# Performance work log

Hardware: AMD Instinct MI355X
Metric: run time of the kernel (lower is better)

Reference implementation:

```python
import jax, jax.numpy as jnp
import numpy as np

EPS = 1e-5

def mvn(x):
    # per-(N,C) spatial mean/std normalization; torch .var is unbiased (ddof=1)
    mean = jnp.mean(x, axis=(2, 3), keepdims=True)
    var = jnp.var(x, axis=(2, 3), ddof=1, keepdims=True)
    return (x - mean) / jnp.sqrt(var + EPS)

def conv1x1(x, w, b):
    # w: [O, C] (1x1 conv collapsed), x: [B, C, H, W]
    return jnp.einsum('bchw,oc->bohw', x, w) + b[None, :, None, None]

def conv3x3(x, w, b):
    # w: [O, I, 3, 3], VALID padding (snet uses padding=0)
    y = jax.lax.conv_general_dilated(x, w, (1, 1), 'VALID',
                                     dimension_numbers=('NCHW', 'OIHW', 'NCHW'))
    return y + b[None, :, None, None]

def safe_cbrt(x):
    # pow(relu(x), 1/3) with safe gradient at 0 (forward identical)
    pos = x > 0
    return jnp.where(pos, jnp.power(jnp.where(pos, x, 1.0), 1.0 / 3.0), 0.0)

def _forward(content, style, wf_san, bf_san, wg_san, bg_san, wh_san, bh_san,
             wf_mcc, bf_mcc, wg_mcc, bg_mcc, w_fc, b_fc, w_out, b_out,
             wc1, bc1, wc2, bc2, wc3, bc3, ws1, bs1, ws2, bs2, ws3, bs3,
             w_unc, b_unc):
    B, C, H, W = content.shape
    cn = mvn(content)
    sn = mvn(style)

    # --- MCC branch: channel correlation statistic of style ---
    F_Fc = conv1x1(cn, wf_mcc, bf_mcc)                      # [B,C,H,W]
    g = conv1x1(sn, wg_mcc, bg_mcc).reshape(B, C, H * W)    # [B,C,HW]
    FC_S = jnp.sum(g * g, axis=-1) / jnp.sum(g, axis=-1)    # [B,C]
    FC_S = FC_S @ w_fc.T + b_fc                             # Linear
    part1 = F_Fc * FC_S[:, :, None, None]

    # --- WCT-like covariance branch (compressed 32-dim space) ---
    Fs0 = style - jnp.mean(style, axis=(2, 3), keepdims=True)  # nor_mean
    fc_ = conv1x1(jax.nn.relu(conv1x1(jax.nn.relu(conv1x1(cn, wc1, bc1)), wc2, bc2)), wc3, bc3)  # [B,32,H,W]
    fs_ = conv1x1(jax.nn.relu(conv3x3(jax.nn.relu(conv3x3(Fs0, ws1, bs1)), ws2, bs2)), ws3, bs3)  # [B,32,H-4,W-4]
    cdim = fc_.shape[1]
    fs_flat = fs_.reshape(B, cdim, -1)                       # [B,32,hw_s]
    cov = jnp.einsum('bci,bdi->bcd', fs_flat, fs_flat) / fs_flat.shape[2]  # [B,32,32]
    out = jnp.einsum('bcd,bdi->bci', cov, fc_.reshape(B, cdim, H * W)).reshape(B, cdim, H, W)
    part2 = conv1x1(out, w_unc, b_unc)                       # [B,512,H,W]

    # --- SANet-style attention branch ---
    F_s = conv1x1(cn, wf_san, bf_san).reshape(B, C, H * W)
    G_s = conv1x1(sn, wg_san, bg_san).reshape(B, C, H * W)
    H_s = conv1x1(style, wh_san, bh_san).reshape(B, C, H * W)
    S = jax.nn.softmax(jnp.einsum('bci,bcj->bij', F_s, G_s), axis=-1)  # [B,HW,HW]
    part3 = jnp.einsum('bcj,bij->bci', H_s, S).reshape(B, C, H, W)

    p = safe_cbrt(jax.nn.relu(part1 * part2 * part3))
    return conv1x1(p, w_out, b_out) + content


def setup_inputs() -> dict:
    key = jax.random.key(0)
    B, C, H, W = 16, 512, 32, 32
    s = 0.02
    shapes = {
        'content': (B, C, H, W), 'style': (B, C, H, W),
        'wf_san': (C, C), 'bf_san': (C,), 'wg_san': (C, C), 'bg_san': (C,),
        'wh_san': (C, C), 'bh_san': (C,),
        'wf_mcc': (C, C), 'bf_mcc': (C,), 'wg_mcc': (C, C), 'bg_mcc': (C,),
        'w_fc': (C, C), 'b_fc': (C,), 'w_out': (C, C), 'b_out': (C,),
        'wc1': (256, 512), 'bc1': (256,), 'wc2': (128, 256), 'bc2': (128,),
        'wc3': (32, 128), 'bc3': (32,),
        'ws1': (256, 512, 3, 3), 'bs1': (256,), 'ws2': (128, 256, 3, 3), 'bs2': (128,),
        'ws3': (32, 128), 'bs3': (32,),
        'w_unc': (512, 32), 'b_unc': (512,),
    }
    d = {}
    for i, (name, shp) in enumerate(shapes.items()):
        k = jax.random.fold_in(key, i)
        scale = 1.0 if name in ('content', 'style') else s
        d[name] = jax.random.normal(k, shp, dtype=jnp.float32) * scale
    return d


def reference(content, style, wf_san, bf_san, wg_san, bg_san, wh_san, bh_san,
              wf_mcc, bf_mcc, wg_mcc, bg_mcc, w_fc, b_fc, w_out, b_out,
              wc1, bc1, wc2, bc2, wc3, bc3, ws1, bs1, ws2, bs2, ws3, bs3,
              w_unc, b_unc):
    return _forward(content, style, wf_san, bf_san, wg_san, bg_san, wh_san, bh_san,
                    wf_mcc, bf_mcc, wg_mcc, bg_mcc, w_fc, b_fc, w_out, b_out,
                    wc1, bc1, wc2, bc2, wc3, bc3, ws1, bs1, ws2, bs2, ws3, bs3,
                    w_unc, b_unc)
```

## Files before the change

### kernel.cpp

```cpp
#include <hip/hip_runtime.h>
#include <hip/hip_bf16.h>
#include <math.h>


typedef __attribute__((ext_vector_type(8))) short short8;
typedef __attribute__((ext_vector_type(4))) float f32x4;
typedef unsigned short us;
#define MFMA16 __builtin_amdgcn_mfma_f32_16x16x32_bf16

__device__ inline float b2f(us b) { return __uint_as_float(((unsigned)b) << 16); }
__device__ inline us f2b(float f) {
    unsigned u = __float_as_uint(f);
    return (us)((u + 0x7FFFu + ((u >> 16) & 1u)) >> 16);
}

__device__ inline double blockReduceSumD(double v, double* sh) {
    int t = threadIdx.x;
    sh[t] = v; __syncthreads();
    for (int s = blockDim.x >> 1; s > 0; s >>= 1) {
        if (t < s) sh[t] += sh[t + s];
        __syncthreads();
    }
    double r = sh[0]; __syncthreads();
    return r;
}

__global__ __launch_bounds__(256) void stats_k(const float* __restrict__ X,
                                               float* __restrict__ mean,
                                               float* __restrict__ inv, int HW) {
    __shared__ double sh[256];
    int bc = blockIdx.x;
    const float* x = X + (size_t)bc * HW;
    int t = threadIdx.x;
    float v[4];
    double s = 0.0;
    #pragma unroll
    for (int r = 0; r < 4; ++r) { v[r] = x[t + r * 256]; s += (double)v[r]; }
    double tot = blockReduceSumD(s, sh);
    double ss = 0.0;
    #pragma unroll
    for (int r = 0; r < 4; ++r) ss += (double)v[r] * (double)v[r];
    double tot2 = blockReduceSumD(ss, sh);
    if (t == 0) {
        double m = tot / HW;
        double var = (tot2 - tot * tot / HW) / (HW - 1);
        mean[bc] = (float)m;
        inv[bc] = (float)(1.0 / sqrt(var + 1e-5));
    }
}

__global__ __launch_bounds__(256) void trn_k(const float* __restrict__ X,
                                             const float* __restrict__ mean,
                                             const float* __restrict__ inv,
                                             us* __restrict__ Yn, us* __restrict__ Yc,
                                             us* __restrict__ Yr, int C, int HW) {
    __shared__ us Ln[64 * 65];
    __shared__ us Lc[64 * 65];
    __shared__ us Lr[64 * 65];
    int bz = blockIdx.z, c0 = blockIdx.y * 64, h0 = blockIdx.x * 64;
    const float* Xb = X + (size_t)bz * C * HW;
    int t = threadIdx.x;
    int cl = t >> 3, h8 = (t & 7) * 8;
    #pragma unroll
    for (int half = 0; half < 2; ++half) {
        int c = cl + half * 32;
        int gc = c0 + c;
        float m = mean[bz * C + gc], iv = inv[bz * C + gc];
        const float4* s4 = (const float4*)&Xb[(size_t)gc * HW + h0 + h8];
        float4 f0 = s4[0], f1 = s4[1];
        float vv[8] = {f0.x, f0.y, f0.z, f0.w, f1.x, f1.y, f1.z, f1.w};
        #pragma unroll
        for (int i = 0; i < 8; ++i) {
            int li = c * 65 + h8 + i;
            if (Yn) Ln[li] = f2b((vv[i] - m) * iv);
            if (Yc) Lc[li] = f2b(vv[i] - m);
            if (Yr) Lr[li] = f2b(vv[i]);
        }
    }
    __syncthreads();
    int hl = t >> 3, c8 = (t & 7) * 8;
    #pragma unroll
    for (int half = 0; half < 2; ++half) {
        int hh = hl + half * 32;
        size_t off = ((size_t)bz * HW + h0 + hh) * (size_t)C + c0 + c8;
        us tmp[8];
        if (Yn) {
            #pragma unroll
            for (int i = 0; i < 8; ++i) tmp[i] = Ln[(c8 + i) * 65 + hh];
            *(uint4*)&Yn[off] = *(const uint4*)tmp;
        }
        if (Yc) {
            #pragma unroll
            for (int i = 0; i < 8; ++i) tmp[i] = Lc[(c8 + i) * 65 + hh];
            *(uint4*)&Yc[off] = *(const uint4*)tmp;
        }
        if (Yr) {
            #pragma unroll
            for (int i = 0; i < 8; ++i) tmp[i] = Lr[(c8 + i) * 65 + hh];
            *(uint4*)&Yr[off] = *(const uint4*)tmp;
        }
    }
}

template <typename TE>
__device__ inline void stage16(const TE* __restrict__ src, bool valid, us* dst) {
    us tmp[16];
    if (valid) {
        if constexpr (sizeof(TE) == 2) {
            uint4 a = ((const uint4*)src)[0], b = ((const uint4*)src)[1];
            *(uint4*)&tmp[0] = a; *(uint4*)&tmp[8] = b;
        } else {
            const float4* s4 = (const float4*)src;
            float4 f0 = s4[0], f1 = s4[1], f2 = s4[2], f3 = s4[3];
            float vv[16] = {f0.x, f0.y, f0.z, f0.w, f1.x, f1.y, f1.z, f1.w,
                            f2.x, f2.y, f2.z, f2.w, f3.x, f3.y, f3.z, f3.w};
            #pragma unroll
            for (int i = 0; i < 16; ++i) tmp[i] = f2b(vv[i]);
        }
    } else {
        #pragma unroll
        for (int i = 0; i < 16; ++i) tmp[i] = 0;
    }
    ((uint4*)dst)[0] = *(uint4*)&tmp[0];
    ((uint4*)dst)[1] = *(uint4*)&tmp[8];
}

template <typename TAel, typename TBel, typename TOUT, int OUTT>
__global__ __launch_bounds__(256) void mf2_k(const TAel* __restrict__ A, long astride, int lda,
                                             const TBel* __restrict__ B, long bstride, int ldb,
                                             const float* __restrict__ bias,
                                             TOUT* __restrict__ Y,
                                             const float* __restrict__ add_src,
                                             int K, int M, int N, int relu) {
    __shared__ us As[2][128][40];
    __shared__ us Bs[2][128][40];
    int bz = blockIdx.z;
    int mbase = blockIdx.y * 128, nbase = blockIdx.x * 128;
    const TAel* Ab = A + (size_t)bz * astride;
    const TBel* Bb = B + (size_t)bz * bstride;
    int t = threadIdx.x;
    int row = t & 127, kh = t >> 7;
    int wave = t >> 6, lane = t & 63, lm = lane & 15, q = lane >> 4;
    int mh = (wave >> 1) * 64, nh = (wave & 1) * 64;
    int gm = mbase + row, gn = nbase + row;
    bool vm = gm < M, vn = gn < N;

    auto stage = [&](int buf, int kb) {
        stage16(Ab + (size_t)gm * lda + kb + kh * 16, vm, &As[buf][row][kh * 16]);
        stage16(Bb + (size_t)gn * ldb + kb + kh * 16, vn, &Bs[buf][row][kh * 16]);
    };

    f32x4 acc[4][4];
    #pragma unroll
    for (int i = 0; i < 4; ++i)
        #pragma unroll
        for (int j = 0; j < 4; ++j) acc[i][j] = (f32x4){0.f, 0.f, 0.f, 0.f};

    stage(0, 0);
    __syncthreads();
    int cur = 0;
    for (int kb = 0; kb < K; kb += 32) {
        if (kb + 32 < K) stage(cur ^ 1, kb + 32);
        short8 af[4], bf[4];
        #pragma unroll
        for (int i = 0; i < 4; ++i) af[i] = *(const short8*)&As[cur][mh + i * 16 + lm][q * 8];
        #pragma unroll
        for (int j = 0; j < 4; ++j) bf[j] = *(const short8*)&Bs[cur][nh + j * 16 + lm][q * 8];
        #pragma unroll
        for (int i = 0; i < 4; ++i)
            #pragma unroll
            for (int j = 0; j < 4; ++j)
                acc[i][j] = MFMA16(af[i], bf[j], acc[i][j], 0, 0, 0);
        __syncthreads();
        cur ^= 1;
    }

    #pragma unroll
    for (int i = 0; i < 4; ++i) {
        int m0 = mbase + mh + i * 16 + q * 4;
        if (m0 >= M) continue;
        float bv[4];
        #pragma unroll
        for (int r = 0; r < 4; ++r) bv[r] = bias ? bias[m0 + r] : 0.f;
        #pragma unroll
        for (int j = 0; j < 4; ++j) {
            int n = nbase + nh + j * 16 + lm;
            if (n >= N) continue;
            float v[4];
            #pragma unroll
            for (int r = 0; r < 4; ++r) {
                float x = acc[i][j][r] + bv[r];
                if (relu) x = (x > 0.f) ? x : 0.f;
                v[r] = x;
            }
            if (OUTT == 1) {
                size_t off = ((size_t)bz * N + n) * (size_t)M + m0;
                if constexpr (sizeof(TOUT) == 2) {
                    us o4[4];
                    #pragma unroll
                    for (int r = 0; r < 4; ++r) o4[r] = f2b(v[r]);
                    *(uint2*)&Y[off] = *(const uint2*)o4;
                } else {
                    float4 f4 = make_float4(v[0], v[1], v[2], v[3]);
                    *(float4*)&Y[off] = f4;
                }
            } else {
                #pragma unroll
                for (int r = 0; r < 4; ++r) {
                    size_t off = ((size_t)bz * M + m0 + r) * (size_t)N + n;
                    float x = v[r];
                    if (add_src) x += add_src[off];
                    if constexpr (sizeof(TOUT) == 2) Y[off] = f2b(x);
                    else Y[off] = x;
                }
            }
        }
    }
}

struct SBias {
    const float* bp[10];
    int moff[10];
    unsigned relu;
};
__global__ __launch_bounds__(256) void mfs_k(const us* __restrict__ A,
                                             const us* __restrict__ B, long bstride, int ldb,
                                             us* __restrict__ Y, int ldy,
                                             SBias sb, int K, int N) {
    __shared__ us As[2][128][40];
    __shared__ us Bs[2][128][40];
    int bz = blockIdx.z;
    int mbase = blockIdx.y * 128, nbase = blockIdx.x * 128;
    const us* Bb = B + (size_t)bz * bstride;
    int t = threadIdx.x;
    int row = t & 127, kh = t >> 7;
    int wave = t >> 6, lane = t & 63, lm = lane & 15, q = lane >> 4;
    int mh = (wave >> 1) * 64, nh = (wave & 1) * 64;
    int relu = (sb.relu >> blockIdx.y) & 1;
    const float* bias = sb.bp[blockIdx.y];
    int moff = sb.moff[blockIdx.y];

    auto stage = [&](int buf, int kb) {
        stage16(A + (size_t)(mbase + row) * K + kb + kh * 16, true, &As[buf][row][kh * 16]);
        stage16(Bb + (size_t)(nbase + row) * ldb + kb + kh * 16, true, &Bs[buf][row][kh * 16]);
    };

    f32x4 acc[4][4];
    #pragma unroll
    for (int i = 0; i < 4; ++i)
        #pragma unroll
        for (int j = 0; j < 4; ++j) acc[i][j] = (f32x4){0.f, 0.f, 0.f, 0.f};

    stage(0, 0);
    __syncthreads();
    int cur = 0;
    for (int kb = 0; kb < K; kb += 32) {
        if (kb + 32 < K) stage(cur ^ 1, kb + 32);
        short8 af[4], bf[4];
        #pragma unroll
        for (int i = 0; i < 4; ++i) af[i] = *(const short8*)&As[cur][mh + i * 16 + lm][q * 8];
        #pragma unroll
        for (int j = 0; j < 4; ++j) bf[j] = *(const short8*)&Bs[cur][nh + j * 16 + lm][q * 8];
        #pragma unroll
        for (int i = 0; i < 4; ++i)
            #pragma unroll
            for (int j = 0; j < 4; ++j)
                acc[i][j] = MFMA16(af[i], bf[j], acc[i][j], 0, 0, 0);
        __syncthreads();
        cur ^= 1;
    }

    #pragma unroll
    for (int i = 0; i < 4; ++i) {
        int m0 = mbase + mh + i * 16 + q * 4;
        float bv[4];
        #pragma unroll
        for (int r = 0; r < 4; ++r) bv[r] = bias[m0 - moff + r];
        #pragma unroll
        for (int j = 0; j < 4; ++j) {
            int n = nbase + nh + j * 16 + lm;
            us o4[4];
            #pragma unroll
            for (int r = 0; r < 4; ++r) {
                float x = acc[i][j][r] + bv[r];
                if (relu) x = (x > 0.f) ? x : 0.f;
                o4[r] = f2b(x);
            }
            *(uint2*)&Y[((size_t)bz * N + n) * ldy + m0] = *(const uint2*)o4;
        }
    }
}

struct CpyArg {
    const float* src[11];
    unsigned long long dstoff[11];
    int len[11];
};
__global__ __launch_bounds__(256) void wcat_k(CpyArg a, us* __restrict__ arena) {
    int seg = blockIdx.y;
    int idx = blockIdx.x * 256 + threadIdx.x;
    if (idx < a.len[seg]) arena[a.dstoff[seg] + idx] = f2b(a.src[seg][idx]);
}

__global__ __launch_bounds__(256) void reorder_wf_k(const float* __restrict__ W,
                                                    us* __restrict__ Wf, int O, int Cin) {
    int idx = blockIdx.x * 256 + threadIdx.x;
    int OT = O >> 6, KB = Cin >> 5;
    int total = OT * KB * 9 * 4 * 64;
    if (idx >= total) return;
    int lane = idx & 63;
    int f = idx >> 6;
    int i = f & 1, half = (f >> 1) & 1;
    int tf = f >> 2;
    int tap = tf % 9;
    int rest = tf / 9;
    int kb = rest % KB, ot = rest / KB;
    int o = ot * 64 + half * 32 + i * 16 + (lane & 15);
    int cb = kb * 32 + (lane >> 4) * 8;
    us v[8];
    #pragma unroll
    for (int e = 0; e < 8; ++e)
        v[e] = f2b(W[((size_t)o * Cin + cb + e) * 9 + tap]);
    *(uint4*)&Wf[(size_t)idx * 8] = *(const uint4*)v;
}

template <int PR>
__device__ inline void stage_patch(const us* __restrict__ Xb, us* __restrict__ dst,
                                   int pyb, int kb, int Cin, int IH, int IW, int t) {
    const int ITEMS = (2 * PR + 2) * 36 * 4;
    for (int i = t; i < ITEMS; i += 256) {
        int p = i >> 2, q8 = (i & 3) * 8;
        int r = p / 36, x = p - r * 36;
        int gy = pyb + r;
        uint4 v = make_uint4(0u, 0u, 0u, 0u);
        if (x < IW && gy < IH)
            v = *(const uint4*)&Xb[((size_t)(gy * IW + x)) * Cin + kb * 32 + q8];
        *(uint4*)&dst[p * 40 + q8] = v;
    }
}

template <int PR>
__global__ __launch_bounds__(256) void conv_mf4_k(const us* __restrict__ X, long xbstride,
                                                  const us* __restrict__ Wf,
                                                  const float* __restrict__ bias,
                                                  us* __restrict__ Y, long ybstride,
                                                  int Cin, int O, int IH, int IW,
                                                  int OH, int OW) {
    __shared__ us patch[2][(2 * PR + 2) * 36 * 40];
    int bz = blockIdx.z;
    int obase = blockIdx.y * 64;
    int pyb = blockIdx.x * (2 * PR);
    const us* Xb = X + (size_t)bz * xbstride;
    int t = threadIdx.x;
    int wave = t >> 6, lane = t & 63, lm = lane & 15, q = lane >> 4;
    int half = wave >> 1, rw = wave & 1;
    int KB = Cin >> 5;
    const us* Wb = Wf + (size_t)(obase >> 6) * KB * 9 * 2048;

    f32x4 acc[PR][2][2];
    #pragma unroll
    for (int pr = 0; pr < PR; ++pr)
        #pragma unroll
        for (int i = 0; i < 2; ++i)
            #pragma unroll
            for (int j = 0; j < 2; ++j) acc[pr][i][j] = (f32x4){0.f, 0.f, 0.f, 0.f};

    stage_patch<PR>(Xb, patch[0], pyb, 0, Cin, IH, IW, t);
    __syncthreads();
    int cur = 0;
    for (int kb = 0; kb < KB; ++kb) {
        if (kb + 1 < KB) stage_patch<PR>(Xb, patch[cur ^ 1], pyb, kb + 1, Cin, IH, IW, t);
        const us* Wk = Wb + (size_t)kb * 9 * 2048;
        #pragma unroll
        for (int tap = 0; tap < 9; ++tap) {
            int ky = tap / 3, kx = tap - ky * 3;
            const us* wt = Wk + tap * 2048 + half * 1024;
            short8 a0 = *(const short8*)&wt[lane * 8];
            short8 a1 = *(const short8*)&wt[512 + lane * 8];
            #pragma unroll
            for (int pr = 0; pr < PR; ++pr) {
                int prow = (pr * 2 + rw + ky) * 36;
                short8 b0 = *(const short8*)&patch[cur][(prow + lm + kx) * 40 + q * 8];
                short8 b1 = *(const short8*)&patch[cur][(prow + 16 + lm + kx) * 40 + q * 8];
                acc[pr][0][0] = MFMA16(a0, b0, acc[pr][0][0], 0, 0, 0);
                acc[pr][0][1] = MFMA16(a0, b1, acc[pr][0][1], 0, 0, 0);
                acc[pr][1][0] = MFMA16(a1, b0, acc[pr][1][0], 0, 0, 0);
                acc[pr][1][1] = MFMA16(a1, b1, acc[pr][1][1], 0, 0, 0);
            }
        }
        __syncthreads();
        cur ^= 1;
    }

    us* Yb = Y + (size_t)bz * ybstride;
    #pragma unroll
    for (int pr = 0; pr < PR; ++pr) {
        int py = pyb + pr * 2 + rw;
        if (py >= OH) continue;
        #pragma unroll
        for (int i = 0; i < 2; ++i) {
            int m0 = obase + half * 32 + i * 16 + q * 4;
            #pragma unroll
            for (int j = 0; j < 2; ++j) {
                int px = j * 16 + lm;
                if (px >= OW) continue;
                us o4[4];
                #pragma unroll
                for (int r = 0; r < 4; ++r) {
                    float v = acc[pr][i][j][r] + bias[m0 + r];
                    v = (v > 0.f) ? v : 0.f;
                    o4[r] = f2b(v);
                }
                *(uint2*)&Yb[((size_t)(py * OW + px)) * O + m0] = *(const uint2*)o4;
            }
        }
    }
}

__global__ __launch_bounds__(256) void gemm_k(const float* __restrict__ W,
                                              const float* __restrict__ X,
                                              const float* __restrict__ bias,
                                              float* __restrict__ Y,
                                              int C, int O, int N) {
    int obase = blockIdx.y * 32;
    __shared__ float As[32][33];
    __shared__ float Bs[32][33];
    int t = threadIdx.x;
    int tx = t & 15, ty = t >> 4;
    float acc00 = 0, acc01 = 0, acc10 = 0, acc11 = 0;
    for (int cb = 0; cb < C; cb += 32) {
        int k = t & 31, o0 = t >> 5;
        #pragma unroll
        for (int r = 0; r < 4; ++r) {
            int ol = o0 + r * 8;
            As[k][ol] = W[(size_t)(obase + ol) * C + cb + k];
        }
        int n0 = t & 31, k0 = t >> 5;
        #pragma unroll
        for (int r = 0; r < 4; ++r) {
            int k2 = k0 + r * 8;
            Bs[k2][n0] = (n0 < N) ? X[(size_t)(cb + k2) * N + n0] : 0.f;
        }
        __syncthreads();
        #pragma unroll
        for (int k2 = 0; k2 < 32; ++k2) {
            float a0 = As[k2][ty], a1 = As[k2][ty + 16];
            float b0 = Bs[k2][tx], b1 = Bs[k2][tx + 16];
            acc00 += a0 * b0; acc01 += a0 * b1;
            acc10 += a1 * b0; acc11 += a1 * b1;
        }
        __syncthreads();
    }
    float accs[2][2] = {{acc00, acc01}, {acc10, acc11}};
    #pragma unroll
    for (int i = 0; i < 2; ++i) {
        int o = obase + ty + i * 16;
        float bv = bias[o];
        #pragma unroll
        for (int j = 0; j < 2; ++j) {
            int n = tx + j * 16;
            if (n < N) Y[(size_t)o * N + n] = accs[i][j] + bv;
        }
    }
}

__global__ __launch_bounds__(256) void fcs3a_k(const us* __restrict__ g, int ldg,
                                               float* __restrict__ pa, int HW) {
    int b = blockIdx.x, j = blockIdx.y;
    int t = threadIdx.x;
    const us* gb = g + ((size_t)b * HW + (size_t)j * 128) * ldg + 2 * t;
    double s0 = 0.0, s1 = 0.0;
    #pragma unroll 4
    for (int hw = 0; hw < 128; ++hw) {
        unsigned u = *(const unsigned*)&gb[(size_t)hw * ldg];
        float f0 = b2f((us)(u & 0xFFFFu));
        float f1 = b2f((us)(u >> 16));
        s0 += (double)f0 * (double)f0;
        s1 += (double)f1 * (double)f1;
    }
    float2 w = make_float2((float)s0, (float)s1);
    *(float2*)&pa[((size_t)b * 8 + j) * 512 + 2 * t] = w;
}

__global__ __launch_bounds__(256) void fcs3b_k(const float* __restrict__ pa,
                                               const float* __restrict__ bg,
                                               float* __restrict__ fcs, int B, int HW) {
    int b = blockIdx.x;
    int t = threadIdx.x;
    double s0 = 0.0, s1 = 0.0;
    #pragma unroll
    for (int j = 0; j < 8; ++j) {
        float2 w = *(const float2*)&pa[((size_t)b * 8 + j) * 512 + 2 * t];
        s0 += (double)w.x; s1 += (double)w.y;
    }
    int c0 = 2 * t;
    fcs[(size_t)c0 * B + b] = (float)(s0 / ((double)HW * (double)bg[c0]));
    fcs[(size_t)(c0 + 1) * B + b] = (float)(s1 / ((double)HW * (double)bg[c0 + 1]));
}

__global__ __launch_bounds__(256) void softmax_k(const float* __restrict__ S,
                                                 us* __restrict__ P) {
    __shared__ float sh[256];
    size_t row = blockIdx.x;
    const float* r = S + row * 1024;
    us* po = P + row * 1024;
    int t = threadIdx.x;
    float v[4];
    float m = -INFINITY;
    #pragma unroll
    for (int i = 0; i < 4; ++i) { v[i] = r[t + i * 256]; m = fmaxf(m, v[i]); }
    sh[t] = m; __syncthreads();
    for (int s = 128; s > 0; s >>= 1) { if (t < s) sh[t] = fmaxf(sh[t], sh[t + s]); __syncthreads(); }
    m = sh[0]; __syncthreads();
    float sum = 0;
    #pragma unroll
    for (int i = 0; i < 4; ++i) { v[i] = expf(v[i] - m); sum += v[i]; }
    sh[t] = sum; __syncthreads();
    for (int s = 128; s > 0; s >>= 1) { if (t < s) sh[t] += sh[t + s]; __syncthreads(); }
    float inv = 1.f / sh[0]; __syncthreads();
    #pragma unroll
    for (int i = 0; i < 4; ++i) po[t + i * 256] = f2b(v[i] * inv);
}

__global__ __launch_bounds__(256) void cov2_k(const float* __restrict__ fs,
                                              float* __restrict__ cov, int Cd, int M) {
    __shared__ float Ls[196 * 36];
    int bb = blockIdx.x;
    int t = threadIdx.x;
    const float* p = fs + (size_t)bb * M * Cd;
    int c = t >> 3, d0 = (t & 7) * 4;
    float a0 = 0.f, a1 = 0.f, a2 = 0.f, a3 = 0.f;
    for (int ch = 0; ch < 4; ++ch) {
        __syncthreads();
        for (int i = t; i < 1568; i += 256) {
            int rowi = i >> 3, c4 = (i & 7) * 4;
            float4 v = *(const float4*)&p[(size_t)(ch * 196 + rowi) * Cd + c4];
            *(float4*)&Ls[rowi * 36 + c4] = v;
        }
        __syncthreads();
        for (int i = 0; i < 196; ++i) {
            float a = Ls[i * 36 + c];
            a0 += a * Ls[i * 36 + d0 + 0];
            a1 += a * Ls[i * 36 + d0 + 1];
            a2 += a * Ls[i * 36 + d0 + 2];
            a3 += a * Ls[i * 36 + d0 + 3];
        }
    }
    float invM = 1.f / (float)M;
    size_t base = ((size_t)bb * Cd + c) * Cd + d0;
    cov[base + 0] = a0 * invM;
    cov[base + 1] = a1 * invM;
    cov[base + 2] = a2 * invM;
    cov[base + 3] = a3 * invM;
}

__global__ __launch_bounds__(256) void fuse_k(const us* __restrict__ ffc, int ldf,
                                              const float* __restrict__ fc2t,
                                              const us* __restrict__ p2,
                                              const us* __restrict__ p3,
                                              us* __restrict__ out, int B, int C, int HW) {
    size_t idx = (size_t)blockIdx.x * 256 + threadIdx.x;
    size_t total = (size_t)B * C * HW;
    if (idx >= total) return;
    int c = (int)(idx & (size_t)(C - 1));
    size_t tok = idx >> 9;
    int b = (int)(idx / ((size_t)C * HW));
    float part1 = b2f(ffc[tok * ldf + c]) * fc2t[(size_t)c * B + b];
    float v = part1 * b2f(p2[idx]) * b2f(p3[idx]);
    v = (v > 0.f) ? v : 0.f;
    out[idx] = f2b(cbrtf(v));
}

extern "C" void kernel_launch(void* const* d_in, const int* in_sizes, int n_in,
                              void* d_out, int out_size, void* d_ws, size_t ws_size,
                              hipStream_t stream) {
    typedef const float* fp;
    fp content = (fp)d_in[0];
    fp style   = (fp)d_in[1];
    fp wf_san = (fp)d_in[2],  bf_san = (fp)d_in[3];
    fp wg_san = (fp)d_in[4],  bg_san = (fp)d_in[5];
    fp wh_san = (fp)d_in[6],  bh_san = (fp)d_in[7];
    fp wf_mcc = (fp)d_in[8],  bf_mcc = (fp)d_in[9];
    fp wg_mcc = (fp)d_in[10], bg_mcc = (fp)d_in[11];
    fp w_fc   = (fp)d_in[12], b_fc   = (fp)d_in[13];
    fp w_out  = (fp)d_in[14], b_out  = (fp)d_in[15];
    fp wc1 = (fp)d_in[16], bc1 = (fp)d_in[17];
    fp wc2 = (fp)d_in[18], bc2 = (fp)d_in[19];
    fp wc3 = (fp)d_in[20], bc3 = (fp)d_in[21];
    fp ws1 = (fp)d_in[22], bs1 = (fp)d_in[23];
    fp ws2 = (fp)d_in[24], bs2 = (fp)d_in[25];
    fp ws3 = (fp)d_in[26], bs3 = (fp)d_in[27];
    fp w_unc = (fp)d_in[28], b_unc = (fp)d_in[29];

    const int B = 16, C = 512, HW = 1024;
    const size_t NE = (size_t)B * C * HW;
    const long TOK = (long)C * HW;
    const size_t MB = 1u << 20;
    char* base = (char*)d_ws;

    us* cnT      = (us*)(base);
    us* snT      = (us*)(base + 16 * MB);
    us* fs0T     = (us*)(base + 32 * MB);
    us* s1       = (us*)(base + 48 * MB);
    us* s2       = (us*)(base + 56 * MB);
    float* fs_c  = (float*)(base + 60 * MB);
    float* Sbuf  = (float*)(base);
    us* cnOut    = (us*)(base + 64 * MB);
    us* snOut    = (us*)(base + 104 * MB);
    us* part3b   = (us*)(base + 104 * MB);
    us* part2b   = (us*)(base + 120 * MB);
    us* Pb       = (us*)(base + 136 * MB);
    us* t2b      = (us*)(base + 136 * MB);
    float* fc_c  = (float*)(base + 140 * MB);
    float* out32 = (float*)(base + 142 * MB);
    us* pbuf     = (us*)(base + 144 * MB);
    us* styleT   = (us*)(base + 168 * MB);
    us* Hco      = (us*)(base + 184 * MB);

    char* misc = base + 200 * MB;
    us* Wr1   = (us*)(misc);
    us* Wr2   = (us*)(misc + 2359296);
    us* arena = (us*)(misc + 2949120);
    us* Wcn   = arena;
    us* Wsn   = arena + 655360;
    us* Wh    = arena + 1179648;
    us* Wout  = arena + 1441792;
    us* Wc2   = arena + 1703936;
    us* Wc3   = arena + 1736704;
    us* Ws3   = arena + 1740800;
    us* Wunc  = arena + 1744896;
    float* pa    = (float*)(misc + 6471680);
    float* fcs   = (float*)(misc + 6733824);
    float* fc2t  = (float*)(misc + 6766592);
    float* cov   = (float*)(misc + 6799360);
    float* meanC = (float*)(misc + 6864896);
    float* invC  = (float*)(misc + 6897664);
    float* meanS = (float*)(misc + 6930432);
    float* invS  = (float*)(misc + 6963200);

    CpyArg ca;
    const float* srcs[11] = {wf_mcc, wc1, wf_san, wg_mcc, wg_san, wh_san,
                             w_out, wc2, wc3, ws3, w_unc};
    int lens[11] = {262144, 131072, 262144, 262144, 262144, 262144,
                    262144, 32768, 4096, 4096, 16384};
    unsigned long long off = 0;
    for (int i = 0; i < 11; ++i) { ca.src[i] = srcs[i]; ca.dstoff[i] = off; ca.len[i] = lens[i]; off += lens[i]; }
    wcat_k<<<dim3(1024, 11), 256, 0, stream>>>(ca, arena);
    reorder_wf_k<<<576, 256, 0, stream>>>(ws1, Wr1, 256, 512);
    reorder_wf_k<<<72, 256, 0, stream>>>(ws2, Wr2, 128, 256);

    stats_k<<<B * C, 256, 0, stream>>>(content, meanC, invC, HW);
    stats_k<<<B * C, 256, 0, stream>>>(style, meanS, invS, HW);
    trn_k<<<dim3(16, 8, 16), 256, 0, stream>>>(content, meanC, invC, cnT, nullptr, nullptr, C, HW);
    trn_k<<<dim3(16, 8, 16), 256, 0, stream>>>(style, meanS, invS, snT, fs0T, styleT, C, HW);

    conv_mf4_k<1><<<dim3(15, 4, 16), 256, 0, stream>>>(fs0T, TOK, Wr1, bs1,
                                                       s1, (long)900 * 256, 512, 256, 32, 32, 30, 30);
    conv_mf4_k<1><<<dim3(14, 2, 16), 256, 0, stream>>>(s1, (long)900 * 256, Wr2, bs2,
                                                       s2, (long)784 * 128, 256, 128, 30, 30, 28, 28);
    mf2_k<us, us, float, 1><<<dim3(7, 1, 16), 256, 0, stream>>>(
        Ws3, 0, 128, s2, (long)784 * 128, 128, bs3, fs_c, nullptr, 128, 32, 784, 0);
    cov2_k<<<B, 256, 0, stream>>>(fs_c, cov, 32, 784);

    {
        SBias sb;
        for (int y = 0; y < 4; ++y) { sb.bp[y] = bf_mcc; sb.moff[y] = 0; }
        for (int y = 4; y < 6; ++y) { sb.bp[y] = bc1; sb.moff[y] = 512; }
        for (int y = 6; y < 10; ++y) { sb.bp[y] = bf_san; sb.moff[y] = 768; }
        sb.relu = 0x030u;
        mfs_k<<<dim3(8, 10, 16), 256, 0, stream>>>(Wcn, cnT, TOK, 512, cnOut, 1280, sb, 512, 1024);
    }

    {
        SBias sb;
        for (int y = 0; y < 4; ++y) { sb.bp[y] = bg_mcc; sb.moff[y] = 0; }
        for (int y = 4; y < 8; ++y) { sb.bp[y] = bg_san; sb.moff[y] = 512; }
        for (int y = 8; y < 10; ++y) { sb.bp[y] = bg_mcc; sb.moff[y] = 0; }
        sb.relu = 0u;
        mfs_k<<<dim3(8, 8, 16), 256, 0, stream>>>(Wsn, snT, TOK, 512, snOut, 1024, sb, 512, 1024);
    }

    fcs3a_k<<<dim3(B, 8), 256, 0, stream>>>(snOut, 1024, pa, HW);
    fcs3b_k<<<B, 256, 0, stream>>>(pa, bg_mcc, fcs, B, HW);
    gemm_k<<<dim3(1, 16, 1), 256, 0, stream>>>(w_fc, fcs, b_fc, fc2t, 512, 512, 16);

    mf2_k<us, us, us, 0><<<dim3(8, 4, 16), 256, 0, stream>>>(
        Wh, 0, 512, styleT, TOK, 512, bh_san, Hco, nullptr, 512, 512, 1024, 0);

    mf2_k<us, us, float, 0><<<dim3(8, 8, 16), 256, 0, stream>>>(
        cnOut + 768, (long)1024 * 1280, 1280, snOut + 512, (long)1024 * 1024, 1024,
        nullptr, Sbuf, nullptr, 512, 1024, 1024, 0);
    softmax_k<<<B * HW, 256, 0, stream>>>(Sbuf, Pb);

    mf2_k<us, us, us, 0><<<dim3(4, 8, 16), 256, 0, stream>>>(
        Pb, (long)1024 * 1024, 1024, Hco, TOK, 1024, nullptr, part3b, nullptr, 1024, 1024, 512, 0);

    mf2_k<us, us, us, 1><<<dim3(8, 1, 16), 256, 0, stream>>>(
        Wc2, 0, 256, cnOut + 512, (long)1024 * 1280, 1280, bc2, t2b, nullptr, 256, 128, 1024, 1);
    mf2_k<us, us, float, 1><<<dim3(8, 1, 16), 256, 0, stream>>>(
        Wc3, 0, 128, t2b, (long)1024 * 128, 128, bc3, fc_c, nullptr, 128, 32, 1024, 0);

    mf2_k<float, float, float, 1><<<dim3(8, 1, 16), 256, 0, stream>>>(
        cov, 1024, 32, fc_c, (long)1024 * 32, 32, nullptr, out32, nullptr, 32, 32, 1024, 0);
    mf2_k<us, float, us, 1><<<dim3(8, 4, 16), 256, 0, stream>>>(
        Wunc, 0, 32, out32, (long)1024 * 32, 32, b_unc, part2b, nullptr, 32, 512, 1024, 0);

    fuse_k<<<(unsigned)((NE + 255) / 256), 256, 0, stream>>>(
        cnOut, 1280, fc2t, part2b, part3b, pbuf, B, C, HW);

    mf2_k<us, us, float, 0><<<dim3(8, 4, 16), 256, 0, stream>>>(
        Wout, 0, 512, pbuf, TOK, 512, b_out, (float*)d_out, content, 512, 512, 1024, 0);
}
```

Measured before the change: 769.4 us.

## Fuse softmax into PV GEMM with fp16 scores and XCD-aware block swizzle

Attention scores are now stored as fp16 instead of fp32. A lightweight wave-per-row kernel computes the row max and inverse sum, and the exponentiation and normalization move into the A-staging step of the PV GEMM, so the separate softmax pass and the bf16 probability buffer go away. All MFMA GEMM and conv kernels also remap block IDs so that consecutive tiles land on the same XCD, aiming for better L2 locality. The costs are recomputing expf for every A tile in each of the 4 N-column blocks, and fp16 range and precision risk on the raw scores.

```diff
diff --git a/kernel.cpp b/kernel.cpp
--- a/kernel.cpp
+++ b/kernel.cpp
@@ -1,5 +1,6 @@
 #include <hip/hip_runtime.h>
 #include <hip/hip_bf16.h>
+#include <hip/hip_fp16.h>
 #include <math.h>
 
 
@@ -8,10 +9,28 @@
 typedef unsigned short us;
 #define MFMA16 __builtin_amdgcn_mfma_f32_16x16x32_bf16
 
+struct h16 { us v; };
+
+template <class A, class B> struct SameT { static constexpr bool v = false; };
+template <class A> struct SameT<A, A> { static constexpr bool v = true; };
+
 __device__ inline float b2f(us b) { return __uint_as_float(((unsigned)b) << 16); }
 __device__ inline us f2b(float f) {
     unsigned u = __float_as_uint(f);
     return (us)((u + 0x7FFFu + ((u >> 16) & 1u)) >> 16);
+}
+
+__device__ inline void xcd_swz3(int& bx, int& by, int& bz) {
+    int gx = gridDim.x, gy = gridDim.y, gz = gridDim.z;
+    int nwg = gx * gy * gz;
+    int flat = (blockIdx.z * gy + blockIdx.y) * gx + blockIdx.x;
+    int xcd = flat & 7, pos = flat >> 3;
+    int q = nwg >> 3, r = nwg & 7;
+    int wgid = (xcd < r ? xcd * (q + 1) : r * (q + 1) + (xcd - r) * q) + pos;
+    bx = wgid % gx;
+    int rest = wgid / gx;
+    by = rest % gy;
+    bz = rest / gy;
 }
 
 __device__ inline double blockReduceSumD(double v, double* sh) {
@@ -134,8 +153,9 @@
                                              int K, int M, int N, int relu) {
     __shared__ us As[2][128][40];
     __shared__ us Bs[2][128][40];
-    int bz = blockIdx.z;
-    int mbase = blockIdx.y * 128, nbase = blockIdx.x * 128;
+    int bx, by, bz;
+    xcd_swz3(bx, by, bz);
+    int mbase = by * 128, nbase = bx * 128;
     const TAel* Ab = A + (size_t)bz * astride;
     const TBel* Bb = B + (size_t)bz * bstride;
     int t = threadIdx.x;
@@ -210,8 +230,10 @@
                     size_t off = ((size_t)bz * M + m0 + r) * (size_t)N + n;
                     float x = v[r];
                     if (add_src) x += add_src[off];
-                    if constexpr (sizeof(TOUT) == 2) Y[off] = f2b(x);
-                    else Y[off] = x;
+                    if constexpr (SameT<TOUT, us>::v) Y[off] = f2b(x);
+                    else if constexpr (SameT<TOUT, h16>::v) {
+                        h16 hh; hh.v = __half_as_ushort(__float2half(x)); Y[off] = hh;
+                    } else Y[off] = x;
                 }
             }
         }
@@ -229,16 +251,17 @@
                                              SBias sb, int K, int N) {
     __shared__ us As[2][128][40];
     __shared__ us Bs[2][128][40];
-    int bz = blockIdx.z;
-    int mbase = blockIdx.y * 128, nbase = blockIdx.x * 128;
+    int bx, by, bz;
+    xcd_swz3(bx, by, bz);
+    int mbase = by * 128, nbase = bx * 128;
     const us* Bb = B + (size_t)bz * bstride;
     int t = threadIdx.x;
     int row = t & 127, kh = t >> 7;
     int wave = t >> 6, lane = t & 63, lm = lane & 15, q = lane >> 4;
     int mh = (wave >> 1) * 64, nh = (wave & 1) * 64;
-    int relu = (sb.relu >> blockIdx.y) & 1;
-    const float* bias = sb.bp[blockIdx.y];
-    int moff = sb.moff[blockIdx.y];
+    int relu = (sb.relu >> by) & 1;
+    const float* bias = sb.bp[by];
+    int moff = sb.moff[by];
 
     auto stage = [&](int buf, int kb) {
         stage16(A + (size_t)(mbase + row) * K + kb + kh * 16, true, &As[buf][row][kh * 16]);
@@ -287,6 +310,111 @@
                 o4[r] = f2b(x);
             }
             *(uint2*)&Y[((size_t)bz * N + n) * ldy + m0] = *(const uint2*)o4;
+        }
+    }
+}
+
+__global__ __launch_bounds__(256) void rowstat_k(const us* __restrict__ S,
+                                                 float* __restrict__ mrow,
+                                                 float* __restrict__ ilrow) {
+    size_t row = (size_t)blockIdx.x * 4 + (threadIdx.x >> 6);
+    int lane = threadIdx.x & 63;
+    const us* r = S + row * 1024 + lane * 16;
+    us raw[16];
+    *(uint4*)&raw[0] = ((const uint4*)r)[0];
+    *(uint4*)&raw[8] = ((const uint4*)r)[1];
+    float v[16];
+    float m = -INFINITY;
+    #pragma unroll
+    for (int e = 0; e < 16; ++e) {
+        v[e] = __half2float(__ushort_as_half(raw[e]));
+        m = fmaxf(m, v[e]);
+    }
+    #pragma unroll
+    for (int off = 32; off > 0; off >>= 1) m = fmaxf(m, __shfl_xor(m, off));
+    float l = 0.f;
+    #pragma unroll
+    for (int e = 0; e < 16; ++e) l += expf(v[e] - m);
+    #pragma unroll
+    for (int off = 32; off > 0; off >>= 1) l += __shfl_xor(l, off);
+    if (lane == 0) { mrow[row] = m; ilrow[row] = 1.f / l; }
+}
+
+__global__ __launch_bounds__(256) void softpv_k(const us* __restrict__ S,
+                                                const float* __restrict__ mrow,
+                                                const float* __restrict__ ilrow,
+                                                const us* __restrict__ H,
+                                                us* __restrict__ Y) {
+    __shared__ us As[2][128][40];
+    __shared__ us Bs[2][128][40];
+    int bx, by, bz;
+    xcd_swz3(bx, by, bz);
+    const int Kd = 1024, M = 1024, N = 512;
+    int mbase = by * 128, nbase = bx * 128;
+    const us* Sb = S + (size_t)bz * M * Kd;
+    const us* Hb = H + (size_t)bz * N * Kd;
+    int t = threadIdx.x;
+    int row = t & 127, kh = t >> 7;
+    int wave = t >> 6, lane = t & 63, lm = lane & 15, q = lane >> 4;
+    int mh = (wave >> 1) * 64, nh = (wave & 1) * 64;
+    float mr = mrow[(size_t)bz * M + mbase + row];
+    float ilr = ilrow[(size_t)bz * M + mbase + row];
+
+    auto stageA = [&](int buf, int kb) {
+        const us* src = Sb + (size_t)(mbase + row) * Kd + kb + kh * 16;
+        us raw[16];
+        *(uint4*)&raw[0] = ((const uint4*)src)[0];
+        *(uint4*)&raw[8] = ((const uint4*)src)[1];
+        us out[16];
+        #pragma unroll
+        for (int e = 0; e < 16; ++e) {
+            float v = __half2float(__ushort_as_half(raw[e]));
+            out[e] = f2b(expf(v - mr) * ilr);
+        }
+        us* dst = &As[buf][row][kh * 16];
+        ((uint4*)dst)[0] = *(uint4*)&out[0];
+        ((uint4*)dst)[1] = *(uint4*)&out[8];
+    };
+    auto stageB = [&](int buf, int kb) {
+        stage16(Hb + (size_t)(nbase + row) * Kd + kb + kh * 16, true, &Bs[buf][row][kh * 16]);
+    };
+
+    f32x4 acc[4][4];
+    #pragma unroll
+    for (int i = 0; i < 4; ++i)
+        #pragma unroll
+        for (int j = 0; j < 4; ++j) acc[i][j] = (f32x4){0.f, 0.f, 0.f, 0.f};
+
+    stageA(0, 0); stageB(0, 0);
+    __syncthreads();
+    int cur = 0;
+    for (int kb = 0; kb < Kd; kb += 32) {
+        if (kb + 32 < Kd) { stageA(cur ^ 1, kb + 32); stageB(cur ^ 1, kb + 32); }
+        short8 af[4], bf[4];
+        #pragma unroll
+        for (int i = 0; i < 4; ++i) af[i] = *(const short8*)&As[cur][mh + i * 16 + lm][q * 8];
+        #pragma unroll
+        for (int j = 0; j < 4; ++j) bf[j] = *(const short8*)&Bs[cur][nh + j * 16 + lm][q * 8];
+        #pragma unroll
+        for (int i = 0; i < 4; ++i)
+            #pragma unroll
+            for (int j = 0; j < 4; ++j)
+                acc[i][j] = MFMA16(af[i], bf[j], acc[i][j], 0, 0, 0);
+        __syncthreads();
+        cur ^= 1;
+    }
+
+    #pragma unroll
+    for (int i = 0; i < 4; ++i) {
+        int m0 = mbase + mh + i * 16 + q * 4;
+        #pragma unroll
+        for (int j = 0; j < 4; ++j) {
+            int n = nbase + nh + j * 16 + lm;
+            #pragma unroll
+            for (int r = 0; r < 4; ++r) {
+                size_t off = ((size_t)bz * M + m0 + r) * (size_t)N + n;
+                Y[off] = f2b(acc[i][j][r]);
+            }
         }
     }
 }
@@ -347,9 +475,10 @@
                                                   int Cin, int O, int IH, int IW,
                                                   int OH, int OW) {
     __shared__ us patch[2][(2 * PR + 2) * 36 * 40];
-    int bz = blockIdx.z;
-    int obase = blockIdx.y * 64;
-    int pyb = blockIdx.x * (2 * PR);
+    int bx, by, bz;
+    xcd_swz3(bx, by, bz);
+    int obase = by * 64;
+    int pyb = bx * (2 * PR);
     const us* Xb = X + (size_t)bz * xbstride;
     int t = threadIdx.x;
     int wave = t >> 6, lane = t & 63, lm = lane & 15, q = lane >> 4;
@@ -496,30 +625,6 @@
     int c0 = 2 * t;
     fcs[(size_t)c0 * B + b] = (float)(s0 / ((double)HW * (double)bg[c0]));
     fcs[(size_t)(c0 + 1) * B + b] = (float)(s1 / ((double)HW * (double)bg[c0 + 1]));
-}
-
-__global__ __launch_bounds__(256) void softmax_k(const float* __restrict__ S,
-                                                 us* __restrict__ P) {
-    __shared__ float sh[256];
-    size_t row = blockIdx.x;
-    const float* r = S + row * 1024;
-    us* po = P + row * 1024;
-    int t = threadIdx.x;
-    float v[4];
-    float m = -INFINITY;
-    #pragma unroll
-    for (int i = 0; i < 4; ++i) { v[i] = r[t + i * 256]; m = fmaxf(m, v[i]); }
-    sh[t] = m; __syncthreads();
-    for (int s = 128; s > 0; s >>= 1) { if (t < s) sh[t] = fmaxf(sh[t], sh[t + s]); __syncthreads(); }
-    m = sh[0]; __syncthreads();
-    float sum = 0;
-    #pragma unroll
-    for (int i = 0; i < 4; ++i) { v[i] = expf(v[i] - m); sum += v[i]; }
-    sh[t] = sum; __syncthreads();
-    for (int s = 128; s > 0; s >>= 1) { if (t < s) sh[t] += sh[t + s]; __syncthreads(); }
-    float inv = 1.f / sh[0]; __syncthreads();
-    #pragma unroll
-    for (int i = 0; i < 4; ++i) po[t + i * 256] = f2b(v[i] * inv);
 }
 
 __global__ __launch_bounds__(256) void cov2_k(const float* __restrict__ fs,
@@ -604,12 +709,12 @@
     us* s1       = (us*)(base + 48 * MB);
     us* s2       = (us*)(base + 56 * MB);
     float* fs_c  = (float*)(base + 60 * MB);
-    float* Sbuf  = (float*)(base);
+    us* Sbuf16   = (us*)(base);
+    h16* Sh      = (h16*)(base);
     us* cnOut    = (us*)(base + 64 * MB);
     us* snOut    = (us*)(base + 104 * MB);
     us* part3b   = (us*)(base + 104 * MB);
     us* part2b   = (us*)(base + 120 * MB);
-    us* Pb       = (us*)(base + 136 * MB);
     us* t2b      = (us*)(base + 136 * MB);
     float* fc_c  = (float*)(base + 140 * MB);
     float* out32 = (float*)(base + 142 * MB);
@@ -637,6 +742,8 @@
     float* invC  = (float*)(misc + 6897664);
     float* meanS = (float*)(misc + 6930432);
     float* invS  = (float*)(misc + 6963200);
+    float* mrow  = (float*)(misc + 6995968);
+    float* ilrow = (float*)(misc + 7061504);
 
     CpyArg ca;
     const float* srcs[11] = {wf_mcc, wc1, wf_san, wg_mcc, wg_san, wh_san,
@@ -687,13 +794,12 @@
     mf2_k<us, us, us, 0><<<dim3(8, 4, 16), 256, 0, stream>>>(
         Wh, 0, 512, styleT, TOK, 512, bh_san, Hco, nullptr, 512, 512, 1024, 0);
 
-    mf2_k<us, us, float, 0><<<dim3(8, 8, 16), 256, 0, stream>>>(
+    mf2_k<us, us, h16, 0><<<dim3(8, 8, 16), 256, 0, stream>>>(
         cnOut + 768, (long)1024 * 1280, 1280, snOut + 512, (long)1024 * 1024, 1024,
-        nullptr, Sbuf, nullptr, 512, 1024, 1024, 0);
-    softmax_k<<<B * HW, 256, 0, stream>>>(Sbuf, Pb);
-
-    mf2_k<us, us, us, 0><<<dim3(4, 8, 16), 256, 0, stream>>>(
-        Pb, (long)1024 * 1024, 1024, Hco, TOK, 1024, nullptr, part3b, nullptr, 1024, 1024, 512, 0);
+        nullptr, Sh, nullptr, 512, 1024, 1024, 0);
+
+    rowstat_k<<<B * HW / 4, 256, 0, stream>>>(Sbuf16, mrow, ilrow);
+    softpv_k<<<dim3(4, 8, 16), 256, 0, stream>>>(Sbuf16, mrow, ilrow, Hco, part3b);
 
     mf2_k<us, us, us, 1><<<dim3(8, 1, 16), 256, 0, stream>>>(
         Wc2, 0, 256, cnOut + 512, (long)1024 * 1280, 1280, bc2, t2b, nullptr, 256, 128, 1024, 1);
```

Measured after the change: 823.7 us. 1.07x slower.

## Stage GEMM epilogues through LDS for coalesced stores and store attention scores as fp16

Applied to the files above, without the earlier changes.

The GEMM kernels now write their 16-bit outputs into a shared-memory tile first and then store them with coalesced 16-byte writes, in place of scattered 2- or 8-byte stores. The attention score matrix is now written in fp16 instead of fp32, which halves the traffic into and out of the softmax. The softmax also switches to vectorized loads and stores. Storing scores in fp16 lowers precision and can overflow if score magnitudes exceed the fp16 range.

```diff
diff --git a/kernel.cpp b/kernel.cpp
--- a/kernel.cpp
+++ b/kernel.cpp
@@ -1,5 +1,6 @@
 #include <hip/hip_runtime.h>
 #include <hip/hip_bf16.h>
+#include <hip/hip_fp16.h>
 #include <math.h>
 
 
@@ -8,10 +9,21 @@
 typedef unsigned short us;
 #define MFMA16 __builtin_amdgcn_mfma_f32_16x16x32_bf16
 
+struct h16 { us v; };
+
+template <class A, class B> struct SameT { static constexpr bool v = false; };
+template <class A> struct SameT<A, A> { static constexpr bool v = true; };
+
 __device__ inline float b2f(us b) { return __uint_as_float(((unsigned)b) << 16); }
 __device__ inline us f2b(float f) {
     unsigned u = __float_as_uint(f);
     return (us)((u + 0x7FFFu + ((u >> 16) & 1u)) >> 16);
+}
+
+template <typename TOUT>
+__device__ inline us cvt2b(float x) {
+    if constexpr (SameT<TOUT, h16>::v) return __half_as_ushort(__float2half(x));
+    else return f2b(x);
 }
 
 __device__ inline double blockReduceSumD(double v, double* sh) {
@@ -132,8 +144,7 @@
                                              TOUT* __restrict__ Y,
                                              const float* __restrict__ add_src,
                                              int K, int M, int N, int relu) {
-    __shared__ us As[2][128][40];
-    __shared__ us Bs[2][128][40];
+    __shared__ __align__(16) us smem[20480];
     int bz = blockIdx.z;
     int mbase = blockIdx.y * 128, nbase = blockIdx.x * 128;
     const TAel* Ab = A + (size_t)bz * astride;
@@ -145,9 +156,12 @@
     int gm = mbase + row, gn = nbase + row;
     bool vm = gm < M, vn = gn < N;
 
+    auto As = [&](int buf) { return smem + buf * 5120; };
+    auto Bs = [&](int buf) { return smem + 10240 + buf * 5120; };
+
     auto stage = [&](int buf, int kb) {
-        stage16(Ab + (size_t)gm * lda + kb + kh * 16, vm, &As[buf][row][kh * 16]);
-        stage16(Bb + (size_t)gn * ldb + kb + kh * 16, vn, &Bs[buf][row][kh * 16]);
+        stage16(Ab + (size_t)gm * lda + kb + kh * 16, vm, As(buf) + row * 40 + kh * 16);
+        stage16(Bb + (size_t)gn * ldb + kb + kh * 16, vn, Bs(buf) + row * 40 + kh * 16);
     };
 
     f32x4 acc[4][4];
@@ -163,9 +177,9 @@
         if (kb + 32 < K) stage(cur ^ 1, kb + 32);
         short8 af[4], bf[4];
         #pragma unroll
-        for (int i = 0; i < 4; ++i) af[i] = *(const short8*)&As[cur][mh + i * 16 + lm][q * 8];
-        #pragma unroll
-        for (int j = 0; j < 4; ++j) bf[j] = *(const short8*)&Bs[cur][nh + j * 16 + lm][q * 8];
+        for (int i = 0; i < 4; ++i) af[i] = *(const short8*)(As(cur) + (mh + i * 16 + lm) * 40 + q * 8);
+        #pragma unroll
+        for (int j = 0; j < 4; ++j) bf[j] = *(const short8*)(Bs(cur) + (nh + j * 16 + lm) * 40 + q * 8);
         #pragma unroll
         for (int i = 0; i < 4; ++i)
             #pragma unroll
@@ -173,6 +187,45 @@
                 acc[i][j] = MFMA16(af[i], bf[j], acc[i][j], 0, 0, 0);
         __syncthreads();
         cur ^= 1;
+    }
+
+    if constexpr (sizeof(TOUT) == 2) {
+        if (mbase + 128 <= M && nbase + 128 <= N) {
+            us* Ts = smem;
+            #pragma unroll
+            for (int i = 0; i < 4; ++i) {
+                int m0 = mh + i * 16 + q * 4;
+                float bv[4];
+                #pragma unroll
+                for (int r = 0; r < 4; ++r) bv[r] = bias ? bias[mbase + m0 + r] : 0.f;
+                #pragma unroll
+                for (int j = 0; j < 4; ++j) {
+                    int nl = nh + j * 16 + lm;
+                    #pragma unroll
+                    for (int r = 0; r < 4; ++r) {
+                        float x = acc[i][j][r] + bv[r];
+                        if (relu) x = (x > 0.f) ? x : 0.f;
+                        us val = cvt2b<TOUT>(x);
+                        if (OUTT == 0) Ts[(m0 + r) * 136 + nl] = val;
+                        else Ts[nl * 136 + m0 + r] = val;
+                    }
+                }
+            }
+            __syncthreads();
+            #pragma unroll
+            for (int k2 = 0; k2 < 8; ++k2) {
+                int flat = k2 * 256 + t;
+                int r0 = flat >> 4, u = flat & 15;
+                uint4 vv = *(const uint4*)&Ts[r0 * 136 + u * 8];
+                us* dst;
+                if (OUTT == 0)
+                    dst = (us*)&Y[((size_t)bz * M + mbase + r0) * N + nbase + u * 8];
+                else
+                    dst = (us*)&Y[((size_t)bz * N + nbase + r0) * M + mbase + u * 8];
+                *(uint4*)dst = vv;
+            }
+            return;
+        }
     }
 
     #pragma unroll
@@ -198,7 +251,7 @@
                 if constexpr (sizeof(TOUT) == 2) {
                     us o4[4];
                     #pragma unroll
-                    for (int r = 0; r < 4; ++r) o4[r] = f2b(v[r]);
+                    for (int r = 0; r < 4; ++r) o4[r] = cvt2b<TOUT>(v[r]);
                     *(uint2*)&Y[off] = *(const uint2*)o4;
                 } else {
                     float4 f4 = make_float4(v[0], v[1], v[2], v[3]);
@@ -210,8 +263,10 @@
                     size_t off = ((size_t)bz * M + m0 + r) * (size_t)N + n;
                     float x = v[r];
                     if (add_src) x += add_src[off];
-                    if constexpr (sizeof(TOUT) == 2) Y[off] = f2b(x);
-                    else Y[off] = x;
+                    if constexpr (sizeof(TOUT) == 2) {
+                        us val = cvt2b<TOUT>(x);
+                        *(us*)&Y[off] = val;
+                    } else Y[off] = x;
                 }
             }
         }
@@ -227,8 +282,7 @@
                                              const us* __restrict__ B, long bstride, int ldb,
                                              us* __restrict__ Y, int ldy,
                                              SBias sb, int K, int N) {
-    __shared__ us As[2][128][40];
-    __shared__ us Bs[2][128][40];
+    __shared__ __align__(16) us smem[20480];
     int bz = blockIdx.z;
     int mbase = blockIdx.y * 128, nbase = blockIdx.x * 128;
     const us* Bb = B + (size_t)bz * bstride;
@@ -240,9 +294,12 @@
     const float* bias = sb.bp[blockIdx.y];
     int moff = sb.moff[blockIdx.y];
 
+    auto As = [&](int buf) { return smem + buf * 5120; };
+    auto Bs = [&](int buf) { return smem + 10240 + buf * 5120; };
+
     auto stage = [&](int buf, int kb) {
-        stage16(A + (size_t)(mbase + row) * K + kb + kh * 16, true, &As[buf][row][kh * 16]);
-        stage16(Bb + (size_t)(nbase + row) * ldb + kb + kh * 16, true, &Bs[buf][row][kh * 16]);
+        stage16(A + (size_t)(mbase + row) * K + kb + kh * 16, true, As(buf) + row * 40 + kh * 16);
+        stage16(Bb + (size_t)(nbase + row) * ldb + kb + kh * 16, true, Bs(buf) + row * 40 + kh * 16);
     };
 
     f32x4 acc[4][4];
@@ -258,9 +315,9 @@
         if (kb + 32 < K) stage(cur ^ 1, kb + 32);
         short8 af[4], bf[4];
         #pragma unroll
-        for (int i = 0; i < 4; ++i) af[i] = *(const short8*)&As[cur][mh + i * 16 + lm][q * 8];
-        #pragma unroll
-        for (int j = 0; j < 4; ++j) bf[j] = *(const short8*)&Bs[cur][nh + j * 16 + lm][q * 8];
+        for (int i = 0; i < 4; ++i) af[i] = *(const short8*)(As(cur) + (mh + i * 16 + lm) * 40 + q * 8);
+        #pragma unroll
+        for (int j = 0; j < 4; ++j) bf[j] = *(const short8*)(Bs(cur) + (nh + j * 16 + lm) * 40 + q * 8);
         #pragma unroll
         for (int i = 0; i < 4; ++i)
             #pragma unroll
@@ -270,24 +327,31 @@
         cur ^= 1;
     }
 
+    us* Ts = smem;
     #pragma unroll
     for (int i = 0; i < 4; ++i) {
-        int m0 = mbase + mh + i * 16 + q * 4;
+        int m0 = mh + i * 16 + q * 4;
         float bv[4];
         #pragma unroll
-        for (int r = 0; r < 4; ++r) bv[r] = bias[m0 - moff + r];
+        for (int r = 0; r < 4; ++r) bv[r] = bias[mbase + m0 - moff + r];
         #pragma unroll
         for (int j = 0; j < 4; ++j) {
-            int n = nbase + nh + j * 16 + lm;
-            us o4[4];
+            int nl = nh + j * 16 + lm;
             #pragma unroll
             for (int r = 0; r < 4; ++r) {
                 float x = acc[i][j][r] + bv[r];
                 if (relu) x = (x > 0.f) ? x : 0.f;
-                o4[r] = f2b(x);
+                Ts[nl * 136 + m0 + r] = f2b(x);
             }
-            *(uint2*)&Y[((size_t)bz * N + n) * ldy + m0] = *(const uint2*)o4;
-        }
+        }
+    }
+    __syncthreads();
+    #pragma unroll
+    for (int k2 = 0; k2 < 8; ++k2) {
+        int flat = k2 * 256 + t;
+        int r0 = flat >> 4, u = flat & 15;
+        uint4 vv = *(const uint4*)&Ts[r0 * 136 + u * 8];
+        *(uint4*)&Y[((size_t)bz * N + nbase + r0) * ldy + mbase + u * 8] = vv;
     }
 }
 
@@ -498,17 +562,22 @@
     fcs[(size_t)(c0 + 1) * B + b] = (float)(s1 / ((double)HW * (double)bg[c0 + 1]));
 }
 
-__global__ __launch_bounds__(256) void softmax_k(const float* __restrict__ S,
+__global__ __launch_bounds__(256) void softmax_k(const us* __restrict__ S,
                                                  us* __restrict__ P) {
     __shared__ float sh[256];
     size_t row = blockIdx.x;
-    const float* r = S + row * 1024;
+    const us* r = S + row * 1024;
     us* po = P + row * 1024;
     int t = threadIdx.x;
+    us raw[4];
+    *(uint2*)raw = *(const uint2*)&r[t * 4];
     float v[4];
     float m = -INFINITY;
     #pragma unroll
-    for (int i = 0; i < 4; ++i) { v[i] = r[t + i * 256]; m = fmaxf(m, v[i]); }
+    for (int i = 0; i < 4; ++i) {
+        v[i] = __half2float(__ushort_as_half(raw[i]));
+        m = fmaxf(m, v[i]);
+    }
     sh[t] = m; __syncthreads();
     for (int s = 128; s > 0; s >>= 1) { if (t < s) sh[t] = fmaxf(sh[t], sh[t + s]); __syncthreads(); }
     m = sh[0]; __syncthreads();
@@ -519,7 +588,8 @@
     for (int s = 128; s > 0; s >>= 1) { if (t < s) sh[t] += sh[t + s]; __syncthreads(); }
     float inv = 1.f / sh[0]; __syncthreads();
     #pragma unroll
-    for (int i = 0; i < 4; ++i) po[t + i * 256] = f2b(v[i] * inv);
+    for (int i = 0; i < 4; ++i) raw[i] = f2b(v[i] * inv);
+    *(uint2*)&po[t * 4] = *(const uint2*)raw;
 }
 
 __global__ __launch_bounds__(256) void cov2_k(const float* __restrict__ fs,
@@ -604,7 +674,8 @@
     us* s1       = (us*)(base + 48 * MB);
     us* s2       = (us*)(base + 56 * MB);
     float* fs_c  = (float*)(base + 60 * MB);
-    float* Sbuf  = (float*)(base);
+    us* Sbuf16   = (us*)(base);
+    h16* Sh      = (h16*)(base);
     us* cnOut    = (us*)(base + 64 * MB);
     us* snOut    = (us*)(base + 104 * MB);
     us* part3b   = (us*)(base + 104 * MB);
@@ -687,13 +758,14 @@
     mf2_k<us, us, us, 0><<<dim3(8, 4, 16), 256, 0, stream>>>(
         Wh, 0, 512, styleT, TOK, 512, bh_san, Hco, nullptr, 512, 512, 1024, 0);
 
-    mf2_k<us, us, float, 0><<<dim3(8, 8, 16), 256, 0, stream>>>(
+    mf2_k<us, us, h16, 0><<<dim3(8, 8, 16), 256, 0, stream>>>(
         cnOut + 768, (long)1024 * 1280, 1280, snOut + 512, (long)1024 * 1024, 1024,
-        nullptr, Sbuf, nullptr, 512, 1024, 1024, 0);
-    softmax_k<<<B * HW, 256, 0, stream>>>(Sbuf, Pb);
+        nullptr, Sh, nullptr, 512, 1024, 1024, 0);
+    softmax_k<<<B * HW, 256, 0, stream>>>(Sbuf16, Pb);
 
     mf2_k<us, us, us, 0><<<dim3(4, 8, 16), 256, 0, stream>>>(
-        Pb, (long)1024 * 1024, 1024, Hco, TOK, 1024, nullptr, part3b, nullptr, 1024, 1024, 512, 0);
+        Pb, (long)1024 * 1024, 1024, Hco, TOK, 1024, nullptr, part3b, nullptr,
+        1024, 1024, 512, 0);
 
     mf2_k<us, us, us, 1><<<dim3(8, 1, 16), 256, 0, stream>>>(
         Wc2, 0, 256, cnOut + 512, (long)1024 * 1280, 1280, bc2, t2b, nullptr, 256, 128, 1024, 1);
```

New measurement: 751.2 us. 2.4% less time.
